# Optimization experiments

Hardware: AMD Instinct MI355X
Metric: run time of the kernel (lower is better)

## Reference

```python
import jax, jax.numpy as jnp
import numpy as np

N_NODES = 50000
N_EDGES = 800000
D_MODEL = 128
N_HEADS = 8
HEAD_DIM = D_MODEL // N_HEADS
EPS = 1e-5


def setup_inputs() -> dict:
    key = jax.random.key(0)
    ks = jax.random.split(key, 8)
    return {
        "node_feature": jax.random.normal(ks[0], (N_NODES, D_MODEL), jnp.float32),
        "dist_attn": jax.random.normal(ks[1], (N_EDGES, N_HEADS), jnp.float32),
        "path_attn": jax.random.normal(ks[2], (N_EDGES, N_HEADS), jnp.float32),
        "gamma": jnp.ones((D_MODEL,), jnp.float32),
        "beta": jnp.zeros((D_MODEL,), jnp.float32),
        "W_qkv": jax.random.normal(ks[3], (3 * D_MODEL, D_MODEL), jnp.float32) * (D_MODEL ** -0.5),
        "b_qkv": jnp.zeros((3 * D_MODEL,), jnp.float32),
        "W_out": jax.random.normal(ks[4], (D_MODEL, D_MODEL), jnp.float32) * (D_MODEL ** -0.5),
        "b_out": jnp.zeros((D_MODEL,), jnp.float32),
        "src": jax.random.randint(ks[5], (N_EDGES,), 0, N_NODES, jnp.int32),
        "dst": jax.random.randint(ks[6], (N_EDGES,), 0, N_NODES, jnp.int32),
    }


def reference(node_feature, dist_attn, path_attn, gamma, beta,
              W_qkv, b_qkv, W_out, b_out, src, dst):
    res = node_feature
    # LayerNorm
    mu = jnp.mean(node_feature, axis=-1, keepdims=True)
    var = jnp.var(node_feature, axis=-1, keepdims=True)
    x = (node_feature - mu) * jax.lax.rsqrt(var + EPS) * gamma + beta
    # QKV projection; scale = d_model**-0.5 (as in source, full d_model)
    qkv = (x @ W_qkv.T + b_qkv).reshape(-1, 3, N_HEADS, HEAD_DIM)
    q = qkv[:, 0] * (D_MODEL ** -0.5)  # [N, H, Dh]
    k = qkv[:, 1]
    v = qkv[:, 2]
    # u_dot_v: dot of src Q with dst K per edge/head -> [E, H]
    node_attn = jnp.einsum("ehd,ehd->eh", q[src], k[dst])
    a = node_attn + dist_attn + path_attn  # [E, H]
    # edge_softmax: segmented softmax over incoming edges of each dst node
    m = jax.ops.segment_max(a, dst, num_segments=N_NODES)  # [N, H]
    ex = jnp.exp(a - m[dst])
    denom = jax.ops.segment_sum(ex, dst, num_segments=N_NODES)  # [N, H]
    sa = ex / denom[dst]  # [E, H]
    # weighted message from src v, summed into dst
    he = v[src] * sa[:, :, None]  # [E, H, Dh]
    agg = jax.ops.segment_sum(he, dst, num_segments=N_NODES)  # [N, H, Dh]
    agg = agg.reshape(-1, D_MODEL)
    out = res + (agg @ W_out.T + b_out)
    return out
```

## Files before the change

### kernel.cpp

```cpp
#include <hip/hip_runtime.h>
#include <math.h>

#define N_NODES 50000
#define N_EDGES 800000
#define D 128
#define NH 8
#define EPS 1e-5f
#define QSCALE 0.08838834764831845f

#define TQ 24
#define TO 8

typedef __attribute__((ext_vector_type(8))) short short8;
typedef __attribute__((ext_vector_type(4))) float f32x4;

__device__ __forceinline__ unsigned short f2bf_rne(float f) {
    unsigned int u = __float_as_uint(f);
    u += 0x7fff + ((u >> 16) & 1);
    return (unsigned short)(u >> 16);
}
__device__ __forceinline__ float bf2f(unsigned short h) {
    return __uint_as_float(((unsigned int)h) << 16);
}
__device__ __forceinline__ float2 bfpair(unsigned int u) {
    return make_float2(__uint_as_float(u << 16),
                       __uint_as_float(u & 0xffff0000u));
}

__device__ __forceinline__ void gload_lds16(const void* g, void* l) {
    __builtin_amdgcn_global_load_lds(
        (const __attribute__((address_space(1))) unsigned int*)g,
        (__attribute__((address_space(3))) unsigned int*)l, 16, 0, 0);
}

__device__ __forceinline__ float qdot(uint4 u, float4 kv) {
    float2 q0 = bfpair(u.x), q1 = bfpair(u.z);
    return q0.x * kv.x + q0.y * kv.y + q1.x * kv.z + q1.y * kv.w;
}
__device__ __forceinline__ void vacc(uint4 u, float w, float& sden,
                                     float& a0, float& a1, float& a2, float& a3) {
    float2 v0 = bfpair(u.y), v1 = bfpair(u.w);
    sden += w;
    a0 += w * v0.x; a1 += w * v0.y; a2 += w * v1.x; a3 += w * v1.y;
}

__global__ void k_prep(const float* __restrict__ Wqkv, const float* __restrict__ Wout,
                       unsigned short* __restrict__ wq_t, unsigned short* __restrict__ wo_t,
                       int* __restrict__ cnt) {
    const int i = blockIdx.x * blockDim.x + threadIdx.x;
    if (i < N_NODES) cnt[i] = 0;
    if (i < TQ * 256) {
        const int nt = i >> 8, r = (i >> 4) & 15, c8 = i & 15;
        const float* s = Wqkv + (size_t)(nt * 16 + r) * D + c8 * 8;
        short8 h8, l8;
        #pragma unroll
        for (int j = 0; j < 8; j++) {
            float w = s[j];
            unsigned short h = f2bf_rne(w);
            h8[j] = (short)h;
            l8[j] = (short)f2bf_rne(w - bf2f(h));
        }
        const int off = (r * 256 + c8 * 16) ^ ((r & 7) << 4);
        char* base = (char*)wq_t + (size_t)nt * 8192;
        *(short8*)(base + off)        = h8;
        *(short8*)(base + 4096 + off) = l8;
    }
    if (i < TO * 256) {
        const int nt = i >> 8, r = (i >> 4) & 15, c8 = i & 15;
        const float* s = Wout + (size_t)(nt * 16 + r) * D + c8 * 8;
        short8 h8, l8;
        #pragma unroll
        for (int j = 0; j < 8; j++) {
            float w = s[j];
            unsigned short h = f2bf_rne(w);
            h8[j] = (short)h;
            l8[j] = (short)f2bf_rne(w - bf2f(h));
        }
        const int off = (r * 256 + c8 * 16) ^ ((r & 7) << 4);
        char* base = (char*)wo_t + (size_t)nt * 8192;
        *(short8*)(base + off)        = h8;
        *(short8*)(base + 4096 + off) = l8;
    }
}

__global__ void k_hist(const int* __restrict__ dst, int* __restrict__ cnt) {
    int e = blockIdx.x * blockDim.x + threadIdx.x;
    if (e < N_EDGES) atomicAdd(&cnt[dst[e]], 1);
}

#define SCB 1024
#define SCG ((N_NODES + SCB - 1) / SCB)

__global__ void k_scan1(const int* __restrict__ cnt, int* __restrict__ row_start,
                        int* __restrict__ bsum) {
    __shared__ int wsum[16];
    const int tid = threadIdx.x, lane = tid & 63, wid = tid >> 6;
    const int gid = blockIdx.x * SCB + tid;
    const int v = (gid < N_NODES) ? cnt[gid] : 0;

    int x = v;
    #pragma unroll
    for (int off = 1; off < 64; off <<= 1) {
        int t = __shfl_up(x, off);
        if (lane >= off) x += t;
    }
    if (lane == 63) wsum[wid] = x;
    __syncthreads();
    if (wid == 0) {
        int w = (lane < 16) ? wsum[lane] : 0;
        #pragma unroll
        for (int off = 1; off < 16; off <<= 1) {
            int t = __shfl_up(w, off);
            if (lane >= off) w += t;
        }
        if (lane < 16) wsum[lane] = w;
    }
    __syncthreads();
    const int base = (wid > 0) ? wsum[wid - 1] : 0;
    const int incl = base + x;
    if (gid < N_NODES) row_start[gid] = incl - v;
    if (tid == SCB - 1) bsum[blockIdx.x] = incl;
}

__global__ void k_scan2(const int* __restrict__ bsum, int* __restrict__ row_start,
                        int* __restrict__ ptrs) {
    __shared__ int boff_s;
    const int tid = threadIdx.x;
    if (tid < 64) {
        int v = (tid < blockIdx.x) ? bsum[tid] : 0;
        #pragma unroll
        for (int off = 1; off < 64; off <<= 1) v += __shfl_xor(v, off);
        if (tid == 0) boff_s = v;
    }
    __syncthreads();
    const int gid = blockIdx.x * SCB + tid;
    if (gid < N_NODES) {
        int r = row_start[gid] + boff_s;
        row_start[gid] = r;
        ptrs[gid] = r;
    }
    if (gid == 0) row_start[N_NODES] = N_EDGES;
}

__global__ void k_fill(const int* __restrict__ src, const int* __restrict__ dst,
                       const float* __restrict__ dist, const float* __restrict__ path,
                       int* __restrict__ ptrs, int* __restrict__ ssrc,
                       float* __restrict__ dp) {
    int e = blockIdx.x * blockDim.x + threadIdx.x;
    if (e < N_EDGES) {
        int d = dst[e];
        int pos = atomicAdd(&ptrs[d], 1);
        ssrc[pos] = src[e];
        #pragma unroll
        for (int h = 0; h < 8; h++)
            dp[(size_t)pos * 8 + h] = dist[(size_t)e * 8 + h] + path[(size_t)e * 8 + h];
    }
}

__launch_bounds__(256)
__global__ void k_ln_qkv(const float* __restrict__ nf, const float* __restrict__ gamma,
                         const float* __restrict__ beta,
                         const unsigned short* __restrict__ wq_t,
                         const float* __restrict__ bqkv,
                         unsigned short* __restrict__ qv, float* __restrict__ kb) {
    __shared__ __align__(16) char lds[2][8192];
    const int lane  = threadIdx.x & 63;
    const int wv    = threadIdx.x >> 6;
    const int nbase = blockIdx.x * 64 + wv * 16;
    const int mrow  = lane & 15;
    const int kg    = lane >> 4;

    int gn = nbase + mrow;
    if (gn >= N_NODES) gn = N_NODES - 1;
    const float* xrow = nf + (size_t)gn * D + kg * 8;
    float4 xa[4], xb[4];
    #pragma unroll
    for (int t = 0; t < 4; t++) {
        xa[t] = *(const float4*)(xrow + t * 32);
        xb[t] = *(const float4*)(xrow + t * 32 + 4);
    }
    float s = 0.f, ss = 0.f;
    #pragma unroll
    for (int t = 0; t < 4; t++) {
        s  += xa[t].x + xa[t].y + xa[t].z + xa[t].w
            + xb[t].x + xb[t].y + xb[t].z + xb[t].w;
        ss += xa[t].x * xa[t].x + xa[t].y * xa[t].y + xa[t].z * xa[t].z + xa[t].w * xa[t].w
            + xb[t].x * xb[t].x + xb[t].y * xb[t].y + xb[t].z * xb[t].z + xb[t].w * xb[t].w;
    }
    s += __shfl_xor(s, 16); ss += __shfl_xor(ss, 16);
    s += __shfl_xor(s, 32); ss += __shfl_xor(ss, 32);
    float mu   = s * (1.f / 128.f);
    float var  = ss * (1.f / 128.f) - mu * mu;
    float rstd = rsqrtf(var + EPS);

    short8 ahi[4], alo[4];
    #pragma unroll
    for (int t = 0; t < 4; t++) {
        const float* gp = gamma + kg * 8 + t * 32;
        const float* bp = beta  + kg * 8 + t * 32;
        float4 g0 = *(const float4*)gp, g1 = *(const float4*)(gp + 4);
        float4 b0 = *(const float4*)bp, b1 = *(const float4*)(bp + 4);
        float xn[8];
        xn[0] = (xa[t].x - mu) * rstd * g0.x + b0.x;
        xn[1] = (xa[t].y - mu) * rstd * g0.y + b0.y;
        xn[2] = (xa[t].z - mu) * rstd * g0.z + b0.z;
        xn[3] = (xa[t].w - mu) * rstd * g0.w + b0.w;
        xn[4] = (xb[t].x - mu) * rstd * g1.x + b1.x;
        xn[5] = (xb[t].y - mu) * rstd * g1.y + b1.y;
        xn[6] = (xb[t].z - mu) * rstd * g1.z + b1.z;
        xn[7] = (xb[t].w - mu) * rstd * g1.w + b1.w;
        #pragma unroll
        for (int j = 0; j < 8; j++) {
            unsigned short h = f2bf_rne(xn[j]);
            ahi[t][j] = (short)h;
            alo[t][j] = (short)f2bf_rne(xn[j] - bf2f(h));
        }
    }

    int boff[4];
    #pragma unroll
    for (int t = 0; t < 4; t++)
        boff[t] = (mrow * 256 + (kg + 4 * t) * 16) ^ ((mrow & 7) << 4);

    {
        const char* g0 = (const char*)wq_t + (size_t)0 * 8192 + wv * 2048 + lane * 16;
        gload_lds16(g0,        lds[0] + wv * 2048);
        gload_lds16(g0 + 1024, lds[0] + wv * 2048 + 1024);
    }
    __syncthreads();

    int cur = 0;
    for (int nt = 0; nt < TQ; ++nt) {
        if (nt + 1 < TQ) {
            const char* g0 = (const char*)wq_t + (size_t)(nt + 1) * 8192 + wv * 2048 + lane * 16;
            gload_lds16(g0,        lds[cur ^ 1] + wv * 2048);
            gload_lds16(g0 + 1024, lds[cur ^ 1] + wv * 2048 + 1024);
        }

        f32x4 acc0 = {0.f, 0.f, 0.f, 0.f};
        f32x4 acc1 = {0.f, 0.f, 0.f, 0.f};
        #pragma unroll
        for (int t = 0; t < 4; t++) {
            short8 bh = *(const short8*)(lds[cur] + boff[t]);
            short8 bl = *(const short8*)(lds[cur] + 4096 + boff[t]);
            acc0 = __builtin_amdgcn_mfma_f32_16x16x32_bf16(ahi[t], bh, acc0, 0, 0, 0);
            acc1 = __builtin_amdgcn_mfma_f32_16x16x32_bf16(alo[t], bh, acc1, 0, 0, 0);
            acc0 = __builtin_amdgcn_mfma_f32_16x16x32_bf16(ahi[t], bl, acc0, 0, 0, 0);
        }

        const int col = nt * 16 + mrow;
        if (nt < 8) {
            float bias = bqkv[col];
            #pragma unroll
            for (int r = 0; r < 4; r++) {
                int node = nbase + kg * 4 + r;
                unsigned int hq = f2bf_rne((acc0[r] + acc1[r] + bias) * QSCALE);
                unsigned int ph = __shfl_xor((int)hq, 1);
                if (!(mrow & 1) && node < N_NODES) {
                    unsigned int u2 = (hq & 0xffffu) | (ph << 16);
                    *(unsigned int*)(qv + (size_t)node * 256 + ((col >> 1) << 2)) = u2;
                }
            }
        } else if (nt < 16) {
            float bias = bqkv[col];
            #pragma unroll
            for (int r = 0; r < 4; r++) {
                int node = nbase + kg * 4 + r;
                if (node < N_NODES)
                    kb[(size_t)node * D + (col - 128)] = acc0[r] + acc1[r] + bias;
            }
        } else {
            float bias = bqkv[col];
            #pragma unroll
            for (int r = 0; r < 4; r++) {
                int node = nbase + kg * 4 + r;
                unsigned int hq = f2bf_rne(acc0[r] + acc1[r] + bias);
                unsigned int ph = __shfl_xor((int)hq, 1);
                if (!(mrow & 1) && node < N_NODES) {
                    unsigned int u2 = (hq & 0xffffu) | (ph << 16);
                    int cv = col - 256;
                    *(unsigned int*)(qv + (size_t)node * 256 + ((cv >> 1) << 2) + 2) = u2;
                }
            }
        }

        __syncthreads();
        cur ^= 1;
    }
}

__launch_bounds__(256, 4)
__global__ void k_gather(const unsigned short* __restrict__ qv,
                         const float* __restrict__ kb,
                         const float* __restrict__ dp,
                         const int* __restrict__ row_start,
                         const int* __restrict__ ssrc,
                         float* __restrict__ agg) {
    const int node = blockIdx.x * 4 + (threadIdx.x >> 6);
    if (node >= N_NODES) return;
    const int lane = threadIdx.x & 63;
    const int half = lane >> 5;
    const int l    = lane & 31;
    const int h    = l >> 2;
    const int beg = row_start[node], end = row_start[node + 1];

    const float4 kv = *(const float4*)(kb + (size_t)node * D + 4 * l);
    float sden = 0.f, a0 = 0.f, a1 = 0.f, a2 = 0.f, a3 = 0.f;

    int i = beg + half;
    for (; i + 6 < end; i += 8) {
        int s0 = ssrc[i], s1 = ssrc[i + 2], s2 = ssrc[i + 4], s3 = ssrc[i + 6];
        uint4 u0 = *(const uint4*)(qv + (size_t)s0 * 256 + l * 8);
        uint4 u1 = *(const uint4*)(qv + (size_t)s1 * 256 + l * 8);
        uint4 u2 = *(const uint4*)(qv + (size_t)s2 * 256 + l * 8);
        uint4 u3 = *(const uint4*)(qv + (size_t)s3 * 256 + l * 8);
        float d0 = dp[(size_t)i * 8 + h];
        float d1 = dp[(size_t)(i + 2) * 8 + h];
        float d2 = dp[(size_t)(i + 4) * 8 + h];
        float d3 = dp[(size_t)(i + 6) * 8 + h];

        float p0 = qdot(u0, kv), p1 = qdot(u1, kv);
        float p2 = qdot(u2, kv), p3 = qdot(u3, kv);
        p0 += __shfl_xor(p0, 1); p1 += __shfl_xor(p1, 1);
        p2 += __shfl_xor(p2, 1); p3 += __shfl_xor(p3, 1);
        p0 += __shfl_xor(p0, 2); p1 += __shfl_xor(p1, 2);
        p2 += __shfl_xor(p2, 2); p3 += __shfl_xor(p3, 2);

        float w0 = __expf(p0 + d0), w1 = __expf(p1 + d1);
        float w2 = __expf(p2 + d2), w3 = __expf(p3 + d3);
        vacc(u0, w0, sden, a0, a1, a2, a3);
        vacc(u1, w1, sden, a0, a1, a2, a3);
        vacc(u2, w2, sden, a0, a1, a2, a3);
        vacc(u3, w3, sden, a0, a1, a2, a3);
    }
    if (i + 2 < end) {
        int s0 = ssrc[i], s1 = ssrc[i + 2];
        uint4 u0 = *(const uint4*)(qv + (size_t)s0 * 256 + l * 8);
        uint4 u1 = *(const uint4*)(qv + (size_t)s1 * 256 + l * 8);
        float d0 = dp[(size_t)i * 8 + h];
        float d1 = dp[(size_t)(i + 2) * 8 + h];
        float p0 = qdot(u0, kv), p1 = qdot(u1, kv);
        p0 += __shfl_xor(p0, 1); p1 += __shfl_xor(p1, 1);
        p0 += __shfl_xor(p0, 2); p1 += __shfl_xor(p1, 2);
        float w0 = __expf(p0 + d0), w1 = __expf(p1 + d1);
        vacc(u0, w0, sden, a0, a1, a2, a3);
        vacc(u1, w1, sden, a0, a1, a2, a3);
        i += 4;
    }
    if (i < end) {
        int s0 = ssrc[i];
        uint4 u0 = *(const uint4*)(qv + (size_t)s0 * 256 + l * 8);
        float d0 = dp[(size_t)i * 8 + h];
        float p0 = qdot(u0, kv);
        p0 += __shfl_xor(p0, 1); p0 += __shfl_xor(p0, 2);
        float w0 = __expf(p0 + d0);
        vacc(u0, w0, sden, a0, a1, a2, a3);
    }

    sden += __shfl_xor(sden, 32);
    a0 += __shfl_xor(a0, 32);
    a1 += __shfl_xor(a1, 32);
    a2 += __shfl_xor(a2, 32);
    a3 += __shfl_xor(a3, 32);

    const float inv = (end > beg) ? 1.f / sden : 0.f;
    if (half == 0) {
        float4 r = make_float4(a0 * inv, a1 * inv, a2 * inv, a3 * inv);
        *(float4*)(agg + (size_t)node * D + 4 * l) = r;
    }
}

__launch_bounds__(256)
__global__ void k_out(const float* __restrict__ agg,
                      const unsigned short* __restrict__ wo_t,
                      const float* __restrict__ bout, const float* __restrict__ nf,
                      float* __restrict__ out) {
    __shared__ __align__(16) char lds[2][8192];
    const int lane  = threadIdx.x & 63;
    const int wv    = threadIdx.x >> 6;
    const int nbase = blockIdx.x * 64 + wv * 16;
    const int mrow  = lane & 15;
    const int kg    = lane >> 4;

    int gn = nbase + mrow;
    if (gn >= N_NODES) gn = N_NODES - 1;
    const float* arow = agg + (size_t)gn * D + kg * 8;

    short8 ahi[4], alo[4];
    #pragma unroll
    for (int t = 0; t < 4; t++) {
        float4 x0 = *(const float4*)(arow + t * 32);
        float4 x1 = *(const float4*)(arow + t * 32 + 4);
        float xn[8] = {x0.x, x0.y, x0.z, x0.w, x1.x, x1.y, x1.z, x1.w};
        #pragma unroll
        for (int j = 0; j < 8; j++) {
            unsigned short h = f2bf_rne(xn[j]);
            ahi[t][j] = (short)h;
            alo[t][j] = (short)f2bf_rne(xn[j] - bf2f(h));
        }
    }

    int boff[4];
    #pragma unroll
    for (int t = 0; t < 4; t++)
        boff[t] = (mrow * 256 + (kg + 4 * t) * 16) ^ ((mrow & 7) << 4);

    {
        const char* g0 = (const char*)wo_t + (size_t)0 * 8192 + wv * 2048 + lane * 16;
        gload_lds16(g0,        lds[0] + wv * 2048);
        gload_lds16(g0 + 1024, lds[0] + wv * 2048 + 1024);
    }
    __syncthreads();

    int cur = 0;
    for (int nt = 0; nt < TO; ++nt) {
        if (nt + 1 < TO) {
            const char* g0 = (const char*)wo_t + (size_t)(nt + 1) * 8192 + wv * 2048 + lane * 16;
            gload_lds16(g0,        lds[cur ^ 1] + wv * 2048);
            gload_lds16(g0 + 1024, lds[cur ^ 1] + wv * 2048 + 1024);
        }

        f32x4 acc0 = {0.f, 0.f, 0.f, 0.f};
        f32x4 acc1 = {0.f, 0.f, 0.f, 0.f};
        #pragma unroll
        for (int t = 0; t < 4; t++) {
            short8 bh = *(const short8*)(lds[cur] + boff[t]);
            short8 bl = *(const short8*)(lds[cur] + 4096 + boff[t]);
            acc0 = __builtin_amdgcn_mfma_f32_16x16x32_bf16(ahi[t], bh, acc0, 0, 0, 0);
            acc1 = __builtin_amdgcn_mfma_f32_16x16x32_bf16(alo[t], bh, acc1, 0, 0, 0);
            acc0 = __builtin_amdgcn_mfma_f32_16x16x32_bf16(ahi[t], bl, acc0, 0, 0, 0);
        }

        const int col = nt * 16 + mrow;
        float bias = bout[col];
        #pragma unroll
        for (int r = 0; r < 4; r++) {
            int node = nbase + kg * 4 + r;
            if (node < N_NODES)
                out[(size_t)node * D + col] =
                    nf[(size_t)node * D + col] + bias + acc0[r] + acc1[r];
        }

        __syncthreads();
        cur ^= 1;
    }
}

extern "C" void kernel_launch(void* const* d_in, const int* in_sizes, int n_in,
                              void* d_out, int out_size, void* d_ws, size_t ws_size,
                              hipStream_t stream) {
    const float* nf    = (const float*)d_in[0];
    const float* dist  = (const float*)d_in[1];
    const float* path  = (const float*)d_in[2];
    const float* gamma = (const float*)d_in[3];
    const float* beta  = (const float*)d_in[4];
    const float* Wqkv  = (const float*)d_in[5];
    const float* bqkv  = (const float*)d_in[6];
    const float* Wout  = (const float*)d_in[7];
    const float* bout  = (const float*)d_in[8];
    const int*   src   = (const int*)d_in[9];
    const int*   dst   = (const int*)d_in[10];
    float* out = (float*)d_out;

    float* kb  = (float*)d_ws;
    float* agg = kb + (size_t)N_NODES * D;
    float* dp  = agg + (size_t)N_NODES * D;
    unsigned short* qvb = (unsigned short*)(dp + (size_t)N_EDGES * 8);
    int* ssrc      = (int*)(qvb + (size_t)N_NODES * 256);
    int* cnt       = ssrc + N_EDGES;
    int* ptrs      = cnt + N_NODES;
    int* row_start = ptrs + N_NODES;
    int* bsum      = row_start + N_NODES + 1;
    uintptr_t p = (uintptr_t)(bsum + 64);
    p = (p + 15) & ~(uintptr_t)15;
    unsigned short* wq_t = (unsigned short*)p;
    unsigned short* wo_t = wq_t + TQ * 4096;

    (void)in_sizes; (void)n_in; (void)out_size; (void)ws_size;

    hipLaunchKernelGGL(k_prep, dim3((N_NODES + 255) / 256), dim3(256), 0, stream,
                       Wqkv, Wout, wq_t, wo_t, cnt);

    hipLaunchKernelGGL(k_hist, dim3((N_EDGES + 255) / 256), dim3(256), 0, stream,
                       dst, cnt);
    hipLaunchKernelGGL(k_scan1, dim3(SCG), dim3(SCB), 0, stream,
                       cnt, row_start, bsum);
    hipLaunchKernelGGL(k_scan2, dim3(SCG), dim3(SCB), 0, stream,
                       bsum, row_start, ptrs);
    hipLaunchKernelGGL(k_fill, dim3((N_EDGES + 255) / 256), dim3(256), 0, stream,
                       src, dst, dist, path, ptrs, ssrc, dp);

    hipLaunchKernelGGL(k_ln_qkv, dim3((N_NODES + 63) / 64), dim3(256), 0, stream,
                       nf, gamma, beta, wq_t, bqkv, qvb, kb);

    hipLaunchKernelGGL(k_gather, dim3((N_NODES + 3) / 4), dim3(256), 0, stream,
                       qvb, kb, dp, row_start, ssrc, agg);

    hipLaunchKernelGGL(k_out, dim3((N_NODES + 63) / 64), dim3(256), 0, stream,
                       agg, wo_t, bout, nf, out);
}
```

Baseline: 215.7 us.

## Record atomic ranks in histogram, drop fill atomics, store edge bias as bf16

The histogram kernel now keeps the rank each atomicAdd returns, so the fill kernel computes scatter positions as row_start plus rank and no longer needs a second pass of atomics or the ptrs copy. Both kernels handle four edges per thread with vector loads. The summed dist+path edge bias is stored as bf16 instead of fp32, which halves its write and its gather-time read. The cost is an extra rank array write and read, plus reduced precision in the pre-softmax bias.

```diff
diff --git a/kernel.cpp b/kernel.cpp
--- a/kernel.cpp
+++ b/kernel.cpp
@@ -83,9 +83,16 @@
     }
 }
 
-__global__ void k_hist(const int* __restrict__ dst, int* __restrict__ cnt) {
-    int e = blockIdx.x * blockDim.x + threadIdx.x;
-    if (e < N_EDGES) atomicAdd(&cnt[dst[e]], 1);
+__global__ void k_hist(const int* __restrict__ dst, int* __restrict__ cnt,
+                       int* __restrict__ rank) {
+    const int e0 = (blockIdx.x * blockDim.x + threadIdx.x) * 4;
+    if (e0 >= N_EDGES) return;
+    const int4 d4 = *(const int4*)(dst + e0);
+    int r0 = atomicAdd(&cnt[d4.x], 1);
+    int r1 = atomicAdd(&cnt[d4.y], 1);
+    int r2 = atomicAdd(&cnt[d4.z], 1);
+    int r3 = atomicAdd(&cnt[d4.w], 1);
+    *(int4*)(rank + e0) = make_int4(r0, r1, r2, r3);
 }
 
 #define SCB 1024
@@ -122,8 +129,7 @@
     if (tid == SCB - 1) bsum[blockIdx.x] = incl;
 }
 
-__global__ void k_scan2(const int* __restrict__ bsum, int* __restrict__ row_start,
-                        int* __restrict__ ptrs) {
+__global__ void k_scan2(const int* __restrict__ bsum, int* __restrict__ row_start) {
     __shared__ int boff_s;
     const int tid = threadIdx.x;
     if (tid < 64) {
@@ -134,26 +140,44 @@
     }
     __syncthreads();
     const int gid = blockIdx.x * SCB + tid;
-    if (gid < N_NODES) {
-        int r = row_start[gid] + boff_s;
-        row_start[gid] = r;
-        ptrs[gid] = r;
-    }
+    if (gid < N_NODES) row_start[gid] += boff_s;
     if (gid == 0) row_start[N_NODES] = N_EDGES;
 }
 
 __global__ void k_fill(const int* __restrict__ src, const int* __restrict__ dst,
+                       const int* __restrict__ rank, const int* __restrict__ row_start,
                        const float* __restrict__ dist, const float* __restrict__ path,
-                       int* __restrict__ ptrs, int* __restrict__ ssrc,
-                       float* __restrict__ dp) {
-    int e = blockIdx.x * blockDim.x + threadIdx.x;
-    if (e < N_EDGES) {
-        int d = dst[e];
-        int pos = atomicAdd(&ptrs[d], 1);
-        ssrc[pos] = src[e];
-        #pragma unroll
-        for (int h = 0; h < 8; h++)
-            dp[(size_t)pos * 8 + h] = dist[(size_t)e * 8 + h] + path[(size_t)e * 8 + h];
+                       int* __restrict__ ssrc, unsigned short* __restrict__ dp16) {
+    const int e0 = (blockIdx.x * blockDim.x + threadIdx.x) * 4;
+    if (e0 >= N_EDGES) return;
+    const int4 s4 = *(const int4*)(src + e0);
+    const int4 d4 = *(const int4*)(dst + e0);
+    const int4 r4 = *(const int4*)(rank + e0);
+    int p0 = row_start[d4.x] + r4.x;
+    int p1 = row_start[d4.y] + r4.y;
+    int p2 = row_start[d4.z] + r4.z;
+    int p3 = row_start[d4.w] + r4.w;
+
+    const int ss[4] = {s4.x, s4.y, s4.z, s4.w};
+    const int pp[4] = {p0, p1, p2, p3};
+    #pragma unroll
+    for (int j = 0; j < 4; j++) {
+        const int e = e0 + j;
+        float4 da = *(const float4*)(dist + (size_t)e * 8);
+        float4 db = *(const float4*)(dist + (size_t)e * 8 + 4);
+        float4 pa = *(const float4*)(path + (size_t)e * 8);
+        float4 pb = *(const float4*)(path + (size_t)e * 8 + 4);
+        short8 w;
+        w[0] = (short)f2bf_rne(da.x + pa.x);
+        w[1] = (short)f2bf_rne(da.y + pa.y);
+        w[2] = (short)f2bf_rne(da.z + pa.z);
+        w[3] = (short)f2bf_rne(da.w + pa.w);
+        w[4] = (short)f2bf_rne(db.x + pb.x);
+        w[5] = (short)f2bf_rne(db.y + pb.y);
+        w[6] = (short)f2bf_rne(db.z + pb.z);
+        w[7] = (short)f2bf_rne(db.w + pb.w);
+        ssrc[pp[j]] = ss[j];
+        *(short8*)(dp16 + (size_t)pp[j] * 8) = w;
     }
 }
 
@@ -292,7 +316,7 @@
 __launch_bounds__(256, 4)
 __global__ void k_gather(const unsigned short* __restrict__ qv,
                          const float* __restrict__ kb,
-                         const float* __restrict__ dp,
+                         const unsigned short* __restrict__ dp16,
                          const int* __restrict__ row_start,
                          const int* __restrict__ ssrc,
                          float* __restrict__ agg) {
@@ -314,10 +338,10 @@
         uint4 u1 = *(const uint4*)(qv + (size_t)s1 * 256 + l * 8);
         uint4 u2 = *(const uint4*)(qv + (size_t)s2 * 256 + l * 8);
         uint4 u3 = *(const uint4*)(qv + (size_t)s3 * 256 + l * 8);
-        float d0 = dp[(size_t)i * 8 + h];
-        float d1 = dp[(size_t)(i + 2) * 8 + h];
-        float d2 = dp[(size_t)(i + 4) * 8 + h];
-        float d3 = dp[(size_t)(i + 6) * 8 + h];
+        float d0 = bf2f(dp16[(size_t)i * 8 + h]);
+        float d1 = bf2f(dp16[(size_t)(i + 2) * 8 + h]);
+        float d2 = bf2f(dp16[(size_t)(i + 4) * 8 + h]);
+        float d3 = bf2f(dp16[(size_t)(i + 6) * 8 + h]);
 
         float p0 = qdot(u0, kv), p1 = qdot(u1, kv);
         float p2 = qdot(u2, kv), p3 = qdot(u3, kv);
@@ -337,8 +361,8 @@
         int s0 = ssrc[i], s1 = ssrc[i + 2];
         uint4 u0 = *(const uint4*)(qv + (size_t)s0 * 256 + l * 8);
         uint4 u1 = *(const uint4*)(qv + (size_t)s1 * 256 + l * 8);
-        float d0 = dp[(size_t)i * 8 + h];
-        float d1 = dp[(size_t)(i + 2) * 8 + h];
+        float d0 = bf2f(dp16[(size_t)i * 8 + h]);
+        float d1 = bf2f(dp16[(size_t)(i + 2) * 8 + h]);
         float p0 = qdot(u0, kv), p1 = qdot(u1, kv);
         p0 += __shfl_xor(p0, 1); p1 += __shfl_xor(p1, 1);
         p0 += __shfl_xor(p0, 2); p1 += __shfl_xor(p1, 2);
@@ -350,7 +374,7 @@
     if (i < end) {
         int s0 = ssrc[i];
         uint4 u0 = *(const uint4*)(qv + (size_t)s0 * 256 + l * 8);
-        float d0 = dp[(size_t)i * 8 + h];
+        float d0 = bf2f(dp16[(size_t)i * 8 + h]);
         float p0 = qdot(u0, kv);
         p0 += __shfl_xor(p0, 1); p0 += __shfl_xor(p0, 2);
         float w0 = __expf(p0 + d0);
@@ -464,12 +488,12 @@
 
     float* kb  = (float*)d_ws;
     float* agg = kb + (size_t)N_NODES * D;
-    float* dp  = agg + (size_t)N_NODES * D;
-    unsigned short* qvb = (unsigned short*)(dp + (size_t)N_EDGES * 8);
-    int* ssrc      = (int*)(qvb + (size_t)N_NODES * 256);
-    int* cnt       = ssrc + N_EDGES;
-    int* ptrs      = cnt + N_NODES;
-    int* row_start = ptrs + N_NODES;
+    unsigned short* qvb  = (unsigned short*)(agg + (size_t)N_NODES * D);
+    unsigned short* dp16 = qvb + (size_t)N_NODES * 256;
+    int* ssrc      = (int*)(dp16 + (size_t)N_EDGES * 8);
+    int* rank      = ssrc + N_EDGES;
+    int* cnt       = rank + N_EDGES;
+    int* row_start = cnt + N_NODES;
     int* bsum      = row_start + N_NODES + 1;
     uintptr_t p = (uintptr_t)(bsum + 64);
     p = (p + 15) & ~(uintptr_t)15;
@@ -481,20 +505,20 @@
     hipLaunchKernelGGL(k_prep, dim3((N_NODES + 255) / 256), dim3(256), 0, stream,
                        Wqkv, Wout, wq_t, wo_t, cnt);
 
-    hipLaunchKernelGGL(k_hist, dim3((N_EDGES + 255) / 256), dim3(256), 0, stream,
-                       dst, cnt);
+    hipLaunchKernelGGL(k_hist, dim3((N_EDGES / 4 + 255) / 256), dim3(256), 0, stream,
+                       dst, cnt, rank);
     hipLaunchKernelGGL(k_scan1, dim3(SCG), dim3(SCB), 0, stream,
                        cnt, row_start, bsum);
     hipLaunchKernelGGL(k_scan2, dim3(SCG), dim3(SCB), 0, stream,
-                       bsum, row_start, ptrs);
-    hipLaunchKernelGGL(k_fill, dim3((N_EDGES + 255) / 256), dim3(256), 0, stream,
-                       src, dst, dist, path, ptrs, ssrc, dp);
+                       bsum, row_start);
+    hipLaunchKernelGGL(k_fill, dim3((N_EDGES / 4 + 255) / 256), dim3(256), 0, stream,
+                       src, dst, rank, row_start, dist, path, ssrc, dp16);
 
     hipLaunchKernelGGL(k_ln_qkv, dim3((N_NODES + 63) / 64), dim3(256), 0, stream,
                        nf, gamma, beta, wq_t, bqkv, qvb, kb);
 
     hipLaunchKernelGGL(k_gather, dim3((N_NODES + 3) / 4), dim3(256), 0, stream,
-                       qvb, kb, dp, row_start, ssrc, agg);
+                       qvb, kb, dp16, row_start, ssrc, agg);
 
     hipLaunchKernelGGL(k_out, dim3((N_NODES + 63) / 64), dim3(256), 0, stream,
                        agg, wo_t, bout, nf, out);
```

After: 204.2 us. 5.3% less time.
